# Performance work log

Measured on AMD Instinct MI355X. Metric: run time of the kernel, lower is better.

The kernel has to match this reference:

```python
import jax, jax.numpy as jnp
import numpy as np

N_NODES = 100000
N_EDGES = 3200000
NUM_FEATURES = 128
NUM_CLASSES = 32
H1, H2 = 64, 32


def _glorot(key, shape):
    lim = float(np.sqrt(6.0 / (shape[0] + shape[1])))
    return jax.random.uniform(key, shape, jnp.float32, -lim, lim)


def setup_inputs() -> dict:
    key = jax.random.key(0)
    ks = jax.random.split(key, 8)
    x = jax.random.normal(ks[0], (N_NODES, NUM_FEATURES), jnp.float32)
    edge_index = jax.random.randint(ks[1], (2, N_EDGES), 0, N_NODES, jnp.int64)
    return {
        "x": x,
        "edge_index": edge_index,
        "W1": _glorot(ks[2], (NUM_FEATURES, H1)), "b1": jnp.zeros((H1,), jnp.float32),
        "W2": _glorot(ks[3], (H1, H2)), "b2": jnp.zeros((H2,), jnp.float32),
        "Wf": _glorot(ks[4], (H2, H2)), "bf": jnp.zeros((H2,), jnp.float32),
        "Wo": _glorot(ks[5], (H2, NUM_CLASSES)), "bo": jnp.zeros((NUM_CLASSES,), jnp.float32),
    }


def gcn_conv(x, src, dst, n, W, b):
    # PyG GCNConv: add self-loops, symmetric normalization D^-1/2 A D^-1/2,
    # aggregate messages source -> target (dst = edge_index[1]).
    h = x @ W                                            # [N, F_out]
    deg = jax.ops.segment_sum(jnp.ones_like(dst, dtype=x.dtype), dst, num_segments=n)
    dinv = jnp.where(deg > 0, jax.lax.rsqrt(deg), 0.0)
    norm = dinv[src] * dinv[dst]                         # [E+N]
    msg = h[src] * norm[:, None]                         # gather + scale
    return jax.ops.segment_sum(msg, dst, num_segments=n) + b


def reference(x, edge_index, W1, b1, W2, b2, Wf, bf, Wo, bo):
    n = x.shape[0]
    loops = jnp.arange(n, dtype=edge_index.dtype)
    src = jnp.concatenate([edge_index[0], loops])
    dst = jnp.concatenate([edge_index[1], loops])
    h = jax.nn.relu(gcn_conv(x, src, dst, n, W1, b1))
    h = gcn_conv(h, src, dst, n, W2, b2)
    h = jax.nn.relu(h @ Wf + bf)
    return h @ Wo + bo
```

## Files before the change

kernel.cpp:

```cpp
#include <hip/hip_runtime.h>
#include <hip/hip_bf16.h>

#define N_NODES 100000
#define N_EDGES 3200000
#define F_IN    128
#define H1F     64
#define H2F     32
#define NCLS    32
#define SCAN_BLOCK 1024
#define SCAN_CHUNKS ((N_NODES + SCAN_BLOCK - 1) / SCAN_BLOCK)
#define NTILES (N_NODES / 16)
#define NCNT   (N_EDGES / 4 / 256)
#define XPAD 132

typedef __attribute__((ext_vector_type(8))) short bf16x8;
typedef __attribute__((ext_vector_type(4))) float f32x4;

static __device__ __forceinline__ float b2f(__hip_bfloat16 v) {
    return __bfloat162float(v);
}
static __device__ __forceinline__ float us2f(unsigned short u) {
    return __uint_as_float(((unsigned)u) << 16);
}
static __device__ __forceinline__ unsigned short f2us(float f) {
    __hip_bfloat16 h = __float2bfloat16(f);
    return *(unsigned short*)&h;
}
static __device__ __forceinline__ float ld(const void* p, size_t i, int isbf) {
    return isbf ? b2f(((const __hip_bfloat16*)p)[i]) : ((const float*)p)[i];
}


__global__ void k_detect(const void* xbuf, const void* eibuf, int* flags) {
    if (threadIdx.x != 0 || blockIdx.x != 0) return;
    const unsigned* ew = (const unsigned*)eibuf;
    int z = 0;
    for (int k = 0; k < 256; ++k) z += (ew[2 * k + 1] == 0u) ? 1 : 0;
    flags[0] = (z >= 200) ? 1 : 0;
    const unsigned* xw = (const unsigned*)xbuf;
    int inr = 0;
    for (int k = 0; k < 256; ++k) {
        unsigned fb = (xw[k] & 0xFFFFu) << 16;
        float a = fabsf(__uint_as_float(fb));
        inr += (a >= 1e-4f && a <= 20.0f) ? 1 : 0;
    }
    flags[1] = (inr >= 160) ? 1 : 0;
}

__global__ void k_packW1(const unsigned short* __restrict__ W1,
                         unsigned short* __restrict__ W1p) {
    int t = blockIdx.x * blockDim.x + threadIdx.x;
    if (t >= F_IN * H1F) return;
    int j    = t & 7;
    int lane = (t >> 3) & 63;
    int fg   = (t >> 9) & 3;
    int kc   = t >> 11;
    int quad = lane >> 4, col = lane & 15;
    W1p[t] = W1[(kc * 32 + quad * 8 + j) * H1F + fg * 16 + col];
}

__global__ void k_dinv(const int* __restrict__ deg, float* __restrict__ dinv) {
    int i = blockIdx.x * blockDim.x + threadIdx.x;
    if (i < N_NODES) dinv[i] = rsqrtf((float)deg[i] + 1.0f);
}

__global__ void k_scanA(const int* __restrict__ deg, int* __restrict__ partial) {
    __shared__ int red[16];
    int b = blockIdx.x, t = threadIdx.x;
    int i = b * SCAN_BLOCK + t;
    int v = (i < N_NODES) ? deg[i] : 0;
    for (int off = 32; off; off >>= 1) v += __shfl_down(v, off, 64);
    if ((t & 63) == 0) red[t >> 6] = v;
    __syncthreads();
    if (t == 0) {
        int s = 0;
        for (int k = 0; k < 16; ++k) s += red[k];
        partial[b] = s;
    }
}

__global__ void k_scanB(const int* __restrict__ partial, int* __restrict__ chunkoff) {
    if (threadIdx.x != 0 || blockIdx.x != 0) return;
    int run = 0;
    for (int b = 0; b < SCAN_CHUNKS; ++b) { chunkoff[b] = run; run += partial[b]; }
}

__global__ void k_scanC(const int* __restrict__ deg, const int* __restrict__ chunkoff,
                        int* __restrict__ rowptr) {
    __shared__ int wsum[16];
    int b = blockIdx.x, t = threadIdx.x, lane = t & 63, w = t >> 6;
    int i = b * SCAN_BLOCK + t;
    int v = (i < N_NODES) ? deg[i] : 0;
    for (int off = 1; off < 64; off <<= 1) {
        int u = __shfl_up(v, off, 64);
        if (lane >= off) v += u;
    }
    if (lane == 63) wsum[w] = v;
    __syncthreads();
    if (t == 0) {
        int run = 0;
        for (int k = 0; k < 16; ++k) { int s = wsum[k]; wsum[k] = run; run += s; }
    }
    __syncthreads();
    int incl = v + wsum[w] + chunkoff[b];
    if (i < N_NODES) rowptr[i + 1] = incl;
    if (b == 0 && t == 0) rowptr[0] = 0;
}

__global__ void k_scatter(const int* __restrict__ ei, const int* __restrict__ aux,
                          const int* __restrict__ rowptr, int* __restrict__ csr,
                          const int* __restrict__ flags) {
    int t = blockIdx.x * blockDim.x + threadIdx.x;
    int e0 = t * 4;
    if (e0 >= N_EDGES) return;
    int s[4], d[4];
    if (flags[0]) {
        const int4* ps = (const int4*)(ei + 2 * (size_t)e0);
        int4 a = ps[0], b = ps[1];
        s[0] = a.x; s[1] = a.z; s[2] = b.x; s[3] = b.z;
        const int4* pd = (const int4*)(ei + 2 * (size_t)(N_EDGES + e0));
        int4 c = pd[0], g = pd[1];
        d[0] = c.x; d[1] = c.z; d[2] = g.x; d[3] = g.z;
    } else {
        int4 a = *(const int4*)(ei + (size_t)e0);
        s[0] = a.x; s[1] = a.y; s[2] = a.z; s[3] = a.w;
        int4 c = *(const int4*)(ei + (size_t)N_EDGES + e0);
        d[0] = c.x; d[1] = c.y; d[2] = c.z; d[3] = c.w;
    }
    int4 av = *(const int4*)(aux + e0);
    int a4[4] = { av.x, av.y, av.z, av.w };
#pragma unroll
    for (int j = 0; j < 4; ++j) {
        if ((unsigned)s[j] < N_NODES && (unsigned)d[j] < N_NODES)
            csr[rowptr[d[j]] + a4[j]] = s[j];
    }
}

__global__ void __launch_bounds__(256)
k_front(const void* __restrict__ x, const void* __restrict__ W1,
        const unsigned short* __restrict__ W1p, const int* __restrict__ ei,
        int* __restrict__ deg, int* __restrict__ aux,
        unsigned short* __restrict__ h1, const int* __restrict__ flags) {
    __shared__ unsigned short w1s[F_IN * H1F];
    __shared__ unsigned short xs[16 * XPAD];
    int blk = blockIdx.x, tid = threadIdx.x;

    if (blk % 3 == 0) {
        int t = (blk / 3) * 256 + tid;
        int e0 = t * 4;
        if (e0 >= N_EDGES) return;
        int d[4];
        if (flags[0]) {
            const int4* p = (const int4*)(ei + 2 * (size_t)(N_EDGES + e0));
            int4 a = p[0], b = p[1];
            d[0] = a.x; d[1] = a.z; d[2] = b.x; d[3] = b.z;
        } else {
            int4 a = *(const int4*)(ei + (size_t)N_EDGES + e0);
            d[0] = a.x; d[1] = a.y; d[2] = a.z; d[3] = a.w;
        }
        int p0 = ((unsigned)d[0] < N_NODES) ? atomicAdd(&deg[d[0]], 1) : 0;
        int p1 = ((unsigned)d[1] < N_NODES) ? atomicAdd(&deg[d[1]], 1) : 0;
        int p2 = ((unsigned)d[2] < N_NODES) ? atomicAdd(&deg[d[2]], 1) : 0;
        int p3 = ((unsigned)d[3] < N_NODES) ? atomicAdd(&deg[d[3]], 1) : 0;
        *(int4*)(aux + e0) = make_int4(p0, p1, p2, p3);
        return;
    }

    int tile = blk - blk / 3 - 1;
    int isbf = flags[1];
    if (isbf) {
        const uint4* src = (const uint4*)W1p;
        uint4*       dst = (uint4*)w1s;
#pragma unroll
        for (int k = 0; k < 4; ++k) dst[tid + k * 256] = src[tid + k * 256];
        const short* xp = (const short*)x + (size_t)tile * 16 * F_IN;
        int r = tid >> 4, c = tid & 15;
        *(bf16x8*)(xs + r * XPAD + c * 8) = *(const bf16x8*)(xp + tid * 8);
    }
    __syncthreads();

    int wave = tid >> 6, lane = tid & 63;
    int col = lane & 15, quad = lane >> 4;
    int fg = wave;

    if (isbf) {
        bf16x8 afr[4];
#pragma unroll
        for (int kc = 0; kc < 4; ++kc)
            afr[kc] = *(const bf16x8*)(xs + col * XPAD + kc * 32 + quad * 8);
        f32x4 acc;
#pragma unroll
        for (int r = 0; r < 4; ++r) acc[r] = 0.f;
#pragma unroll
        for (int kc = 0; kc < 4; ++kc) {
            bf16x8 bfr = *(const bf16x8*)(w1s + (((kc * 4 + fg) * 64 + lane) * 8));
            acc = __builtin_amdgcn_mfma_f32_16x16x32_bf16(afr[kc], bfr, acc, 0, 0, 0);
        }
#pragma unroll
        for (int r = 0; r < 4; ++r)
            h1[(size_t)(tile * 16 + quad * 4 + r) * H1F + fg * 16 + col] = f2us(acc[r]);
    } else {
        const float* wfp = (const float*)W1;
        for (int i = 0; i < 4; ++i) {
            int n = tile * 16 + wave * 4 + i;
            const float2* xr = (const float2*)((const float*)x + (size_t)n * F_IN);
            float2 my = xr[lane];
            float acc = 0.f;
#pragma unroll 16
            for (int k = 0; k < 64; ++k) {
                float x0 = __shfl(my.x, k, 64);
                float x1 = __shfl(my.y, k, 64);
                acc += x0 * wfp[(2 * k) * H1F + lane];
                acc += x1 * wfp[(2 * k + 1) * H1F + lane];
            }
            h1[(size_t)n * H1F + lane] = f2us(acc);
        }
    }
}

__global__ void k_agg1gemm2(const unsigned short* __restrict__ h1,
                            const float* __restrict__ dinv,
                            const int* __restrict__ rowptr, const int* __restrict__ csr,
                            const void* __restrict__ b1, const void* __restrict__ W2,
                            unsigned short* __restrict__ h2, const int* __restrict__ flags) {
    int n    = (blockIdx.x * blockDim.x + threadIdx.x) >> 6;
    int lane = threadIdx.x & 63;
    if (n >= N_NODES) return;
    int beg = rowptr[n], end = rowptr[n + 1];
    float dn  = dinv[n];
    float acc = dn * us2f(h1[(size_t)n * H1F + lane]);
    int e = beg;
    for (; e + 3 < end; e += 4) {
        int s0 = csr[e], s1 = csr[e + 1], s2 = csr[e + 2], s3 = csr[e + 3];
        float w0 = dinv[s0], w1 = dinv[s1], w2 = dinv[s2], w3 = dinv[s3];
        unsigned short v0 = h1[(size_t)s0 * H1F + lane];
        unsigned short v1 = h1[(size_t)s1 * H1F + lane];
        unsigned short v2 = h1[(size_t)s2 * H1F + lane];
        unsigned short v3 = h1[(size_t)s3 * H1F + lane];
        acc += w0 * us2f(v0) + w1 * us2f(v1) + w2 * us2f(v2) + w3 * us2f(v3);
    }
    for (; e < end; ++e) {
        int s = csr[e];
        acc += dinv[s] * us2f(h1[(size_t)s * H1F + lane]);
    }
    acc *= dn;
    int isbf = flags[1];
    float bv = isbf ? b2f(((const __hip_bfloat16*)b1)[lane]) : ((const float*)b1)[lane];
    float v  = fmaxf(acc + bv, 0.f);
    int f = lane & 31, h = lane >> 5;
    float part = 0.f;
    if (isbf) {
        const __hip_bfloat16* w = (const __hip_bfloat16*)W2;
#pragma unroll
        for (int j = 0; j < 32; ++j) {
            int k = h * 32 + j;
            part += __shfl(v, k, 64) * b2f(w[k * H2F + f]);
        }
    } else {
        const float* w = (const float*)W2;
#pragma unroll
        for (int j = 0; j < 32; ++j) {
            int k = h * 32 + j;
            part += __shfl(v, k, 64) * w[k * H2F + f];
        }
    }
    part += __shfl(part, lane ^ 32, 64);
    if (h == 0) h2[(size_t)n * H2F + f] = f2us(part);
}

__global__ void GCN_51737176048479_kernel(const unsigned short* __restrict__ h2,
                                          const float* __restrict__ dinv,
                                          const int* __restrict__ rowptr,
                                          const int* __restrict__ csr,
                                          const void* __restrict__ b2v,
                                          const void* __restrict__ Wf,
                                          const void* __restrict__ bfv,
                                          const void* __restrict__ Wo,
                                          const void* __restrict__ bov,
                                          void* __restrict__ out,
                                          const int* __restrict__ flags) {
    int tid = blockIdx.x * blockDim.x + threadIdx.x;
    int n   = tid >> 5;
    int f   = threadIdx.x & 31;
    if (n >= N_NODES) return;
    int isbf = flags[1];
    int beg = rowptr[n], end = rowptr[n + 1];
    float dn = dinv[n];
    float ar = dn * us2f(h2[(size_t)n * H2F + f]);
    int e = beg;
    for (; e + 3 < end; e += 4) {
        int s0 = csr[e], s1 = csr[e + 1], s2 = csr[e + 2], s3 = csr[e + 3];
        float w0 = dinv[s0], w1 = dinv[s1], w2 = dinv[s2], w3 = dinv[s3];
        unsigned short v0 = h2[(size_t)s0 * H2F + f];
        unsigned short v1 = h2[(size_t)s1 * H2F + f];
        unsigned short v2 = h2[(size_t)s2 * H2F + f];
        unsigned short v3 = h2[(size_t)s3 * H2F + f];
        ar += w0 * us2f(v0) + w1 * us2f(v1) + w2 * us2f(v2) + w3 * us2f(v3);
    }
    for (; e < end; ++e) {
        int s = csr[e];
        ar += dinv[s] * us2f(h2[(size_t)s * H2F + f]);
    }
    ar = ar * dn + ld(b2v, f, isbf);
    float acc1 = 0.f;
#pragma unroll
    for (int k = 0; k < H2F; ++k)
        acc1 += __shfl(ar, k, 32) * ld(Wf, (size_t)k * H2F + f, isbf);
    float u = fmaxf(acc1 + ld(bfv, f, isbf), 0.f);
    float acc2 = 0.f;
#pragma unroll
    for (int k = 0; k < H2F; ++k)
        acc2 += __shfl(u, k, 32) * ld(Wo, (size_t)k * NCLS + f, isbf);
    float r = acc2 + ld(bov, f, isbf);
    size_t oi = (size_t)n * NCLS + f;
    if (isbf) ((__hip_bfloat16*)out)[oi] = __float2bfloat16(r);
    else      ((float*)out)[oi] = r;
}

extern "C" void kernel_launch(void* const* d_in, const int* in_sizes, int n_in,
                              void* d_out, int out_size, void* d_ws, size_t ws_size,
                              hipStream_t stream) {
    const void* x  = d_in[0];
    const int*  ei = (const int*)d_in[1];
    const void* W1 = d_in[2];
    const void* b1 = d_in[3];
    const void* W2 = d_in[4];
    const void* b2 = d_in[5];
    const void* Wf = d_in[6];
    const void* bf = d_in[7];
    const void* Wo = d_in[8];
    const void* bo = d_in[9];

    char* ws = (char*)d_ws;
    int*            deg      = (int*)  (ws + 0);
    int*            rowptr   = (int*)  (ws + (512u  << 10));
    float*          dinv     = (float*)(ws + (1024u << 10));
    int*            flags    = (int*)  (ws + (1434u << 10));
    int*            partial  = (int*)  (ws + (1444u << 10));
    int*            chunkoff = (int*)  (ws + (1454u << 10));
    unsigned short* W1p      = (unsigned short*)(ws + (1536u << 10));
    int*            aux      = (int*)  (ws + (2u  << 20));
    int*            csr      = (int*)  (ws + (15u << 20));
    unsigned short* h1       = (unsigned short*)(ws + (28u << 20));
    unsigned short* h2       = (unsigned short*)(ws + (41u << 20));

    const int B = 256;

    k_detect<<<1, 64, 0, stream>>>(x, ei, flags);
    hipMemsetAsync(deg, 0, N_NODES * sizeof(int), stream);
    k_packW1<<<(F_IN * H1F + B - 1) / B, B, 0, stream>>>((const unsigned short*)W1, W1p);

    k_front<<<NTILES + NCNT, B, 0, stream>>>(x, W1, W1p, ei, deg, aux, h1, flags);

    k_dinv<<<(N_NODES + B - 1) / B, B, 0, stream>>>(deg, dinv);
    k_scanA<<<SCAN_CHUNKS, SCAN_BLOCK, 0, stream>>>(deg, partial);
    k_scanB<<<1, 64, 0, stream>>>(partial, chunkoff);
    k_scanC<<<SCAN_CHUNKS, SCAN_BLOCK, 0, stream>>>(deg, chunkoff, rowptr);
    k_scatter<<<(N_EDGES / 4 + B - 1) / B, B, 0, stream>>>(ei, aux, rowptr, csr, flags);

    k_agg1gemm2<<<(N_NODES * 64 + B - 1) / B, B, 0, stream>>>(h1, dinv, rowptr, csr,
                                                              b1, W2, h2, flags);
    GCN_51737176048479_kernel<<<(N_NODES * 32 + B - 1) / B, B, 0, stream>>>(
        h2, dinv, rowptr, csr, b2, Wf, bf, Wo, bo, d_out, flags);
}
```

Before: 599.7 us.

## Replace CSR build with fixed-slot adjacency plus overflow list

Drops the degree scan, dinv, and scatter kernels and instead writes each edge's source directly into a per-destination fixed array of 80 slots during the degree-counting atomics. Edges beyond the slot capacity go to a global overflow list that every aggregation thread scans linearly. dinv is recomputed on the fly from deg. This removes several launches and the second pass over edges, but the layout depends on degrees staying below 80 (true for these random inputs, with mean degree 32), and the overflow scan would be very expensive if many overflow entries existed.

Result: slower. 624.8 us (+4.2%).

```diff
diff --git a/kernel.cpp b/kernel.cpp
--- a/kernel.cpp
+++ b/kernel.cpp
@@ -7,11 +7,11 @@
 #define H1F     64
 #define H2F     32
 #define NCLS    32
-#define SCAN_BLOCK 1024
-#define SCAN_CHUNKS ((N_NODES + SCAN_BLOCK - 1) / SCAN_BLOCK)
 #define NTILES (N_NODES / 16)
 #define NCNT   (N_EDGES / 4 / 256)
 #define XPAD 132
+#define SLOTS 80
+#define OVCAP 65536
 
 typedef __attribute__((ext_vector_type(8))) short bf16x8;
 typedef __attribute__((ext_vector_type(4))) float f32x4;
@@ -28,6 +28,9 @@
 }
 static __device__ __forceinline__ float ld(const void* p, size_t i, int isbf) {
     return isbf ? b2f(((const __hip_bfloat16*)p)[i]) : ((const float*)p)[i];
+}
+static __device__ __forceinline__ float dinvf(int dg) {
+    return rsqrtf((float)dg + 1.0f);
 }
 
 
@@ -59,87 +62,11 @@
     W1p[t] = W1[(kc * 32 + quad * 8 + j) * H1F + fg * 16 + col];
 }
 
-__global__ void k_dinv(const int* __restrict__ deg, float* __restrict__ dinv) {
-    int i = blockIdx.x * blockDim.x + threadIdx.x;
-    if (i < N_NODES) dinv[i] = rsqrtf((float)deg[i] + 1.0f);
-}
-
-__global__ void k_scanA(const int* __restrict__ deg, int* __restrict__ partial) {
-    __shared__ int red[16];
-    int b = blockIdx.x, t = threadIdx.x;
-    int i = b * SCAN_BLOCK + t;
-    int v = (i < N_NODES) ? deg[i] : 0;
-    for (int off = 32; off; off >>= 1) v += __shfl_down(v, off, 64);
-    if ((t & 63) == 0) red[t >> 6] = v;
-    __syncthreads();
-    if (t == 0) {
-        int s = 0;
-        for (int k = 0; k < 16; ++k) s += red[k];
-        partial[b] = s;
-    }
-}
-
-__global__ void k_scanB(const int* __restrict__ partial, int* __restrict__ chunkoff) {
-    if (threadIdx.x != 0 || blockIdx.x != 0) return;
-    int run = 0;
-    for (int b = 0; b < SCAN_CHUNKS; ++b) { chunkoff[b] = run; run += partial[b]; }
-}
-
-__global__ void k_scanC(const int* __restrict__ deg, const int* __restrict__ chunkoff,
-                        int* __restrict__ rowptr) {
-    __shared__ int wsum[16];
-    int b = blockIdx.x, t = threadIdx.x, lane = t & 63, w = t >> 6;
-    int i = b * SCAN_BLOCK + t;
-    int v = (i < N_NODES) ? deg[i] : 0;
-    for (int off = 1; off < 64; off <<= 1) {
-        int u = __shfl_up(v, off, 64);
-        if (lane >= off) v += u;
-    }
-    if (lane == 63) wsum[w] = v;
-    __syncthreads();
-    if (t == 0) {
-        int run = 0;
-        for (int k = 0; k < 16; ++k) { int s = wsum[k]; wsum[k] = run; run += s; }
-    }
-    __syncthreads();
-    int incl = v + wsum[w] + chunkoff[b];
-    if (i < N_NODES) rowptr[i + 1] = incl;
-    if (b == 0 && t == 0) rowptr[0] = 0;
-}
-
-__global__ void k_scatter(const int* __restrict__ ei, const int* __restrict__ aux,
-                          const int* __restrict__ rowptr, int* __restrict__ csr,
-                          const int* __restrict__ flags) {
-    int t = blockIdx.x * blockDim.x + threadIdx.x;
-    int e0 = t * 4;
-    if (e0 >= N_EDGES) return;
-    int s[4], d[4];
-    if (flags[0]) {
-        const int4* ps = (const int4*)(ei + 2 * (size_t)e0);
-        int4 a = ps[0], b = ps[1];
-        s[0] = a.x; s[1] = a.z; s[2] = b.x; s[3] = b.z;
-        const int4* pd = (const int4*)(ei + 2 * (size_t)(N_EDGES + e0));
-        int4 c = pd[0], g = pd[1];
-        d[0] = c.x; d[1] = c.z; d[2] = g.x; d[3] = g.z;
-    } else {
-        int4 a = *(const int4*)(ei + (size_t)e0);
-        s[0] = a.x; s[1] = a.y; s[2] = a.z; s[3] = a.w;
-        int4 c = *(const int4*)(ei + (size_t)N_EDGES + e0);
-        d[0] = c.x; d[1] = c.y; d[2] = c.z; d[3] = c.w;
-    }
-    int4 av = *(const int4*)(aux + e0);
-    int a4[4] = { av.x, av.y, av.z, av.w };
-#pragma unroll
-    for (int j = 0; j < 4; ++j) {
-        if ((unsigned)s[j] < N_NODES && (unsigned)d[j] < N_NODES)
-            csr[rowptr[d[j]] + a4[j]] = s[j];
-    }
-}
-
 __global__ void __launch_bounds__(256)
 k_front(const void* __restrict__ x, const void* __restrict__ W1,
         const unsigned short* __restrict__ W1p, const int* __restrict__ ei,
-        int* __restrict__ deg, int* __restrict__ aux,
+        int* __restrict__ deg, int* __restrict__ csrF,
+        int* __restrict__ novf, int2* __restrict__ ov,
         unsigned short* __restrict__ h1, const int* __restrict__ flags) {
     __shared__ unsigned short w1s[F_IN * H1F];
     __shared__ unsigned short xs[16 * XPAD];
@@ -149,20 +76,34 @@
         int t = (blk / 3) * 256 + tid;
         int e0 = t * 4;
         if (e0 >= N_EDGES) return;
-        int d[4];
+        int s[4], d[4];
         if (flags[0]) {
-            const int4* p = (const int4*)(ei + 2 * (size_t)(N_EDGES + e0));
-            int4 a = p[0], b = p[1];
-            d[0] = a.x; d[1] = a.z; d[2] = b.x; d[3] = b.z;
+            const int4* ps = (const int4*)(ei + 2 * (size_t)e0);
+            int4 a = ps[0], b = ps[1];
+            s[0] = a.x; s[1] = a.z; s[2] = b.x; s[3] = b.z;
+            const int4* pd = (const int4*)(ei + 2 * (size_t)(N_EDGES + e0));
+            int4 c = pd[0], g = pd[1];
+            d[0] = c.x; d[1] = c.z; d[2] = g.x; d[3] = g.z;
         } else {
-            int4 a = *(const int4*)(ei + (size_t)N_EDGES + e0);
-            d[0] = a.x; d[1] = a.y; d[2] = a.z; d[3] = a.w;
-        }
-        int p0 = ((unsigned)d[0] < N_NODES) ? atomicAdd(&deg[d[0]], 1) : 0;
-        int p1 = ((unsigned)d[1] < N_NODES) ? atomicAdd(&deg[d[1]], 1) : 0;
-        int p2 = ((unsigned)d[2] < N_NODES) ? atomicAdd(&deg[d[2]], 1) : 0;
-        int p3 = ((unsigned)d[3] < N_NODES) ? atomicAdd(&deg[d[3]], 1) : 0;
-        *(int4*)(aux + e0) = make_int4(p0, p1, p2, p3);
+            int4 a = *(const int4*)(ei + (size_t)e0);
+            s[0] = a.x; s[1] = a.y; s[2] = a.z; s[3] = a.w;
+            int4 c = *(const int4*)(ei + (size_t)N_EDGES + e0);
+            d[0] = c.x; d[1] = c.y; d[2] = c.z; d[3] = c.w;
+        }
+#pragma unroll
+        for (int j = 0; j < 4; ++j) {
+            if ((unsigned)d[j] < N_NODES) {
+                int r = atomicAdd(&deg[d[j]], 1);
+                if ((unsigned)s[j] < N_NODES) {
+                    if (r < SLOTS) {
+                        csrF[(size_t)d[j] * SLOTS + r] = s[j];
+                    } else {
+                        int o = atomicAdd(novf, 1);
+                        if (o < OVCAP) ov[o] = make_int2(d[j], s[j]);
+                    }
+                }
+            }
+        }
         return;
     }
 
@@ -219,20 +160,24 @@
 }
 
 __global__ void k_agg1gemm2(const unsigned short* __restrict__ h1,
-                            const float* __restrict__ dinv,
-                            const int* __restrict__ rowptr, const int* __restrict__ csr,
+                            const int* __restrict__ deg,
+                            const int* __restrict__ csrF,
+                            const int* __restrict__ novf, const int2* __restrict__ ov,
                             const void* __restrict__ b1, const void* __restrict__ W2,
                             unsigned short* __restrict__ h2, const int* __restrict__ flags) {
     int n    = (blockIdx.x * blockDim.x + threadIdx.x) >> 6;
     int lane = threadIdx.x & 63;
     if (n >= N_NODES) return;
-    int beg = rowptr[n], end = rowptr[n + 1];
-    float dn  = dinv[n];
+    int dg  = deg[n];
+    int end = dg < SLOTS ? dg : SLOTS;
+    const int* row = csrF + (size_t)n * SLOTS;
+    float dn  = dinvf(dg);
     float acc = dn * us2f(h1[(size_t)n * H1F + lane]);
-    int e = beg;
+    int e = 0;
     for (; e + 3 < end; e += 4) {
-        int s0 = csr[e], s1 = csr[e + 1], s2 = csr[e + 2], s3 = csr[e + 3];
-        float w0 = dinv[s0], w1 = dinv[s1], w2 = dinv[s2], w3 = dinv[s3];
+        int s0 = row[e], s1 = row[e + 1], s2 = row[e + 2], s3 = row[e + 3];
+        float w0 = dinvf(deg[s0]), w1 = dinvf(deg[s1]);
+        float w2 = dinvf(deg[s2]), w3 = dinvf(deg[s3]);
         unsigned short v0 = h1[(size_t)s0 * H1F + lane];
         unsigned short v1 = h1[(size_t)s1 * H1F + lane];
         unsigned short v2 = h1[(size_t)s2 * H1F + lane];
@@ -240,8 +185,13 @@
         acc += w0 * us2f(v0) + w1 * us2f(v1) + w2 * us2f(v2) + w3 * us2f(v3);
     }
     for (; e < end; ++e) {
-        int s = csr[e];
-        acc += dinv[s] * us2f(h1[(size_t)s * H1F + lane]);
+        int s = row[e];
+        acc += dinvf(deg[s]) * us2f(h1[(size_t)s * H1F + lane]);
+    }
+    int nov = *novf; nov = nov < OVCAP ? nov : OVCAP;
+    for (int i = 0; i < nov; ++i) {
+        int2 p = ov[i];
+        if (p.x == n) acc += dinvf(deg[p.y]) * us2f(h1[(size_t)p.y * H1F + lane]);
     }
     acc *= dn;
     int isbf = flags[1];
@@ -269,9 +219,10 @@
 }
 
 __global__ void GCN_51737176048479_kernel(const unsigned short* __restrict__ h2,
-                                          const float* __restrict__ dinv,
-                                          const int* __restrict__ rowptr,
-                                          const int* __restrict__ csr,
+                                          const int* __restrict__ deg,
+                                          const int* __restrict__ csrF,
+                                          const int* __restrict__ novf,
+                                          const int2* __restrict__ ov,
                                           const void* __restrict__ b2v,
                                           const void* __restrict__ Wf,
                                           const void* __restrict__ bfv,
@@ -284,13 +235,16 @@
     int f   = threadIdx.x & 31;
     if (n >= N_NODES) return;
     int isbf = flags[1];
-    int beg = rowptr[n], end = rowptr[n + 1];
-    float dn = dinv[n];
+    int dg  = deg[n];
+    int end = dg < SLOTS ? dg : SLOTS;
+    const int* row = csrF + (size_t)n * SLOTS;
+    float dn = dinvf(dg);
     float ar = dn * us2f(h2[(size_t)n * H2F + f]);
-    int e = beg;
+    int e = 0;
     for (; e + 3 < end; e += 4) {
-        int s0 = csr[e], s1 = csr[e + 1], s2 = csr[e + 2], s3 = csr[e + 3];
-        float w0 = dinv[s0], w1 = dinv[s1], w2 = dinv[s2], w3 = dinv[s3];
+        int s0 = row[e], s1 = row[e + 1], s2 = row[e + 2], s3 = row[e + 3];
+        float w0 = dinvf(deg[s0]), w1 = dinvf(deg[s1]);
+        float w2 = dinvf(deg[s2]), w3 = dinvf(deg[s3]);
         unsigned short v0 = h2[(size_t)s0 * H2F + f];
         unsigned short v1 = h2[(size_t)s1 * H2F + f];
         unsigned short v2 = h2[(size_t)s2 * H2F + f];
@@ -298,8 +252,13 @@
         ar += w0 * us2f(v0) + w1 * us2f(v1) + w2 * us2f(v2) + w3 * us2f(v3);
     }
     for (; e < end; ++e) {
-        int s = csr[e];
-        ar += dinv[s] * us2f(h2[(size_t)s * H2F + f]);
+        int s = row[e];
+        ar += dinvf(deg[s]) * us2f(h2[(size_t)s * H2F + f]);
+    }
+    int nov = *novf; nov = nov < OVCAP ? nov : OVCAP;
+    for (int i = 0; i < nov; ++i) {
+        int2 p = ov[i];
+        if (p.x == n) ar += dinvf(deg[p.y]) * us2f(h2[(size_t)p.y * H2F + f]);
     }
     ar = ar * dn + ld(b2v, f, isbf);
     float acc1 = 0.f;
@@ -332,34 +291,26 @@
     const void* bo = d_in[9];
 
     char* ws = (char*)d_ws;
-    int*            deg      = (int*)  (ws + 0);
-    int*            rowptr   = (int*)  (ws + (512u  << 10));
-    float*          dinv     = (float*)(ws + (1024u << 10));
-    int*            flags    = (int*)  (ws + (1434u << 10));
-    int*            partial  = (int*)  (ws + (1444u << 10));
-    int*            chunkoff = (int*)  (ws + (1454u << 10));
-    unsigned short* W1p      = (unsigned short*)(ws + (1536u << 10));
-    int*            aux      = (int*)  (ws + (2u  << 20));
-    int*            csr      = (int*)  (ws + (15u << 20));
-    unsigned short* h1       = (unsigned short*)(ws + (28u << 20));
-    unsigned short* h2       = (unsigned short*)(ws + (41u << 20));
+    int*            deg   = (int*)  (ws + 0);
+    int*            novf  = (int*)  (ws + 400000);
+    int*            flags = (int*)  (ws + (512u << 10));
+    int2*           ov    = (int2*) (ws + (520u << 10));
+    unsigned short* W1p   = (unsigned short*)(ws + (1536u << 10));
+    int*            csrF  = (int*)  (ws + (2u  << 20));
+    unsigned short* h1    = (unsigned short*)(ws + (35u << 20));
+    unsigned short* h2    = (unsigned short*)(ws + (48u << 20));
 
     const int B = 256;
 
     k_detect<<<1, 64, 0, stream>>>(x, ei, flags);
-    hipMemsetAsync(deg, 0, N_NODES * sizeof(int), stream);
+    hipMemsetAsync(deg, 0, 400000 + 4, stream);
     k_packW1<<<(F_IN * H1F + B - 1) / B, B, 0, stream>>>((const unsigned short*)W1, W1p);
 
-    k_front<<<NTILES + NCNT, B, 0, stream>>>(x, W1, W1p, ei, deg, aux, h1, flags);
-
-    k_dinv<<<(N_NODES + B - 1) / B, B, 0, stream>>>(deg, dinv);
-    k_scanA<<<SCAN_CHUNKS, SCAN_BLOCK, 0, stream>>>(deg, partial);
-    k_scanB<<<1, 64, 0, stream>>>(partial, chunkoff);
-    k_scanC<<<SCAN_CHUNKS, SCAN_BLOCK, 0, stream>>>(deg, chunkoff, rowptr);
-    k_scatter<<<(N_EDGES / 4 + B - 1) / B, B, 0, stream>>>(ei, aux, rowptr, csr, flags);
-
-    k_agg1gemm2<<<(N_NODES * 64 + B - 1) / B, B, 0, stream>>>(h1, dinv, rowptr, csr,
+    k_front<<<NTILES + NCNT, B, 0, stream>>>(x, W1, W1p, ei, deg, csrF, novf, ov,
+                                             h1, flags);
+
+    k_agg1gemm2<<<(N_NODES * 64 + B - 1) / B, B, 0, stream>>>(h1, deg, csrF, novf, ov,
                                                               b1, W2, h2, flags);
     GCN_51737176048479_kernel<<<(N_NODES * 32 + B - 1) / B, B, 0, stream>>>(
-        h2, dinv, rowptr, csr, b2, Wf, bf, Wo, bo, d_out, flags);
-}
+        h2, deg, csrF, novf, ov, b2, Wf, bf, Wo, bo, d_out, flags);
+}
```
